# Kernel optimization log

Hardware: AMD Instinct MI355X
Metric: run time of the kernel (lower is better)

The kernel has to match this reference:

```python
import jax, jax.numpy as jnp
import numpy as np

N_HEAD = 16
D_MODEL = 1024
D_HEAD = D_MODEL // N_HEAD  # 64
B, S = 1, 4096


def setup_inputs() -> dict:
    key = jax.random.key(0)
    ks = jax.random.split(key, 7)
    q = jax.random.normal(ks[0], (B, S, D_MODEL), dtype=jnp.float32)
    k = jax.random.normal(ks[1], (B, S, D_MODEL), dtype=jnp.float32)
    v = jax.random.normal(ks[2], (B, S, D_MODEL), dtype=jnp.float32)
    mask = jnp.ones((S, S), dtype=bool)
    # params match torch.rand init (uniform [0,1)); use uniform here too
    w_q = jax.random.uniform(ks[3], (D_MODEL, D_MODEL), dtype=jnp.float32)
    w_k = jax.random.uniform(ks[4], (D_HEAD, D_MODEL), dtype=jnp.float32)
    w_v = jax.random.uniform(ks[5], (D_HEAD, D_MODEL), dtype=jnp.float32)
    w_out = jax.random.uniform(ks[6], (D_MODEL, D_MODEL), dtype=jnp.float32)
    return {"q": q, "k": k, "v": v, "mask": mask,
            "w_q": w_q, "w_k": w_k, "w_v": w_v, "w_out": w_out}


def reference(q, k, v, mask, w_q, w_k, w_v, w_out):
    # F.linear(x, W) == x @ W.T
    query = q @ w_q.T                      # [b, n, d_model]
    key = k @ w_k.T                        # [b, s, d_head]  (single shared KV head)
    value = v @ w_v.T                      # [b, s, d_head]
    b, n, _ = query.shape
    query = query.reshape(b, n, N_HEAD, D_HEAD).transpose(0, 2, 1, 3)  # b h n d
    scores = jnp.einsum('bhnd,bsd->bhns', query, key) / jnp.sqrt(jnp.float32(D_HEAD))
    scores = jnp.where(mask[None, None], scores, jnp.float32(-jnp.inf))
    attn = jax.nn.softmax(scores, axis=-1)             # [b, h, n, s]
    out = jnp.einsum('bhns,bsd->bhnd', attn, value)    # [b, h, n, d]
    out = out.transpose(0, 2, 1, 3).reshape(b, n, D_MODEL)
    return out @ w_out.T
```

## Files before the change

kernel.cpp:

```cpp
#include <hip/hip_runtime.h>
#include <cstdint>
#include <cstddef>

#define S_LEN   4096
#define DM      1024
#define NHEAD   16
#define DH      64

typedef short bf16x8 __attribute__((ext_vector_type(8)));
typedef _Float16 f16x8 __attribute__((ext_vector_type(8)));
typedef float f32x4  __attribute__((ext_vector_type(4)));

__device__ __forceinline__ unsigned short f2bf(float x) {
    uint32_t u = __float_as_uint(x);
    u += 0x7fffu + ((u >> 16) & 1u);
    return (unsigned short)(u >> 16);
}
__device__ __forceinline__ float bf2f(unsigned short u) {
    return __uint_as_float(((uint32_t)u) << 16);
}
__device__ __forceinline__ unsigned pack_bf2(float a, float b) {
    return (unsigned)f2bf(a) | ((unsigned)f2bf(b) << 16);
}
__device__ __forceinline__ unsigned short f2h(float x) {
    _Float16 h = (_Float16)x;
    return __builtin_bit_cast(unsigned short, h);
}
__device__ __forceinline__ unsigned pack_h2(float a, float b) {
    return __builtin_bit_cast(unsigned, __builtin_amdgcn_cvt_pkrtz(a, b));
}
__device__ __forceinline__ void gl_lds16(const unsigned short* g, unsigned short* l) {
    __builtin_amdgcn_global_load_lds(
        (const __attribute__((address_space(1))) unsigned int*)g,
        (__attribute__((address_space(3))) unsigned int*)l, 16, 0, 0);
}

__global__ void cvt_all(const float* __restrict__ q, const float* __restrict__ k,
                        const float* __restrict__ v, const float* __restrict__ wq,
                        const float* __restrict__ wk, const float* __restrict__ wv,
                        const float* __restrict__ wo,
                        unsigned short* __restrict__ qh, unsigned short* __restrict__ ql,
                        unsigned short* __restrict__ kh, unsigned short* __restrict__ kl,
                        unsigned short* __restrict__ vh,
                        unsigned short* __restrict__ wqh, unsigned short* __restrict__ wql,
                        unsigned short* __restrict__ wkh, unsigned short* __restrict__ wkl,
                        unsigned short* __restrict__ wvh, unsigned short* __restrict__ woh)
{
    const int G1 = 1048576, GW = 262144, GK = 16384;
    int i = blockIdx.x * blockDim.x + threadIdx.x;
    const float* src; unsigned short* h; unsigned short* l = nullptr; int off;
    if (i < 3 * G1) {
        if (i < G1)            { src = q; h = qh; l = ql; off = i; }
        else if (i < 2 * G1)   { src = k; h = kh; l = kl; off = i - G1; }
        else                   { src = v; h = vh;         off = i - 2 * G1; }
    } else {
        int j = i - 3 * G1;
        if (j < GW)            { src = wq; h = wqh; l = wql; off = j; }
        else if (j < GW + GK)  { src = wk; h = wkh; l = wkl; off = j - GW; }
        else if (j < GW + 2*GK){ src = wv; h = wvh;          off = j - GW - GK; }
        else                   { src = wo; h = woh;          off = j - GW - 2 * GK; }
    }
    float4 vv = reinterpret_cast<const float4*>(src)[off];
    ushort4 hh;
    hh.x = f2bf(vv.x); hh.y = f2bf(vv.y); hh.z = f2bf(vv.z); hh.w = f2bf(vv.w);
    reinterpret_cast<ushort4*>(h)[off] = hh;
    if (l) {
        ushort4 ll;
        ll.x = f2bf(vv.x - bf2f(hh.x)); ll.y = f2bf(vv.y - bf2f(hh.y));
        ll.z = f2bf(vv.z - bf2f(hh.z)); ll.w = f2bf(vv.w - bf2f(hh.w));
        reinterpret_cast<ushort4*>(l)[off] = ll;
    }
}

template<int TERMS, int MODE>
__launch_bounds__(256)
__global__ void gemm_bt(const unsigned short* __restrict__ Ah,
                        const unsigned short* __restrict__ Al,
                        const unsigned short* __restrict__ Bh,
                        const unsigned short* __restrict__ Bl,
                        unsigned short* __restrict__ Ch,
                        unsigned short* __restrict__ Cl,
                        float* __restrict__ Cf,
                        int M, int N, int K, int ldc)
{
    __shared__ unsigned short As_h[64][72];
    __shared__ unsigned short Bs_h[64][72];
    __shared__ unsigned short As_l[TERMS == 3 ? 64 : 1][72];
    __shared__ unsigned short Bs_l[TERMS == 3 ? 64 : 1][72];

    const int tid  = threadIdx.x;
    const int wave = tid >> 6;
    const int lane = tid & 63;
    const int lm   = lane & 15;
    const int quad = lane >> 4;
    const int m0   = blockIdx.x * 64;
    const int n0   = blockIdx.y * 64;

    f32x4 acc[4] = {};

    for (int kc = 0; kc < K; kc += 64) {
#pragma unroll
        for (int i = 0; i < 2; ++i) {
            int c   = tid + i * 256;
            int r   = c >> 3;
            int col = (c & 7) * 8;
            *(uint4*)&As_h[r][col] = *(const uint4*)&Ah[(size_t)(m0 + r) * K + kc + col];
            *(uint4*)&Bs_h[r][col] = *(const uint4*)&Bh[(size_t)(n0 + r) * K + kc + col];
            if (TERMS == 3) {
                *(uint4*)&As_l[r][col] = *(const uint4*)&Al[(size_t)(m0 + r) * K + kc + col];
                *(uint4*)&Bs_l[r][col] = *(const uint4*)&Bl[(size_t)(n0 + r) * K + kc + col];
            }
        }
        __syncthreads();
#pragma unroll
        for (int kk = 0; kk < 64; kk += 32) {
            bf16x8 bh = *(const bf16x8*)&Bs_h[wave * 16 + lm][kk + quad * 8];
            bf16x8 bl;
            if (TERMS == 3) bl = *(const bf16x8*)&Bs_l[wave * 16 + lm][kk + quad * 8];
#pragma unroll
            for (int ms = 0; ms < 4; ++ms) {
                bf16x8 ah = *(const bf16x8*)&As_h[ms * 16 + lm][kk + quad * 8];
                acc[ms] = __builtin_amdgcn_mfma_f32_16x16x32_bf16(ah, bh, acc[ms], 0, 0, 0);
                if (TERMS == 3) {
                    bf16x8 al = *(const bf16x8*)&As_l[ms * 16 + lm][kk + quad * 8];
                    acc[ms] = __builtin_amdgcn_mfma_f32_16x16x32_bf16(ah, bl, acc[ms], 0, 0, 0);
                    acc[ms] = __builtin_amdgcn_mfma_f32_16x16x32_bf16(al, bh, acc[ms], 0, 0, 0);
                }
            }
        }
        __syncthreads();
    }

#pragma unroll
    for (int ms = 0; ms < 4; ++ms) {
#pragma unroll
        for (int r = 0; r < 4; ++r) {
            int row = m0 + ms * 16 + quad * 4 + r;
            int col = n0 + wave * 16 + lm;
            float v = acc[ms][r];
            if (MODE == 0) {
                unsigned short h = f2bf(v);
                Ch[(size_t)row * ldc + col] = h;
                Cl[(size_t)row * ldc + col] = f2bf(v - bf2f(h));
            } else if (MODE == 2) {
                Cf[(size_t)row * ldc + col] = v;
            } else if (MODE == 3) {
                Ch[(size_t)row * ldc + col] = f2h(v);
            } else if (MODE == 4) {
                Ch[(size_t)col * ldc + row] = f2h(v);
            }
        }
    }
}

template<int TERMS, int MODE>
__launch_bounds__(256)
__global__ void gemm_big(const unsigned short* __restrict__ Ah,
                         const unsigned short* __restrict__ Al,
                         const unsigned short* __restrict__ Bh,
                         const unsigned short* __restrict__ Bl,
                         unsigned short* __restrict__ Ch,
                         unsigned short* __restrict__ Cl,
                         float* __restrict__ Cf,
                         int M, int N, int K, int ldc)
{
    __shared__ unsigned short As_h[2][8192];
    __shared__ unsigned short Bs_h[2][8192];
    __shared__ unsigned short As_l[TERMS == 3 ? 2 : 1][TERMS == 3 ? 8192 : 1];
    __shared__ unsigned short Bs_l[TERMS == 3 ? 2 : 1][TERMS == 3 ? 8192 : 1];

    const int tid  = threadIdx.x;
    const int wave = tid >> 6;
    const int lane = tid & 63;
    const int lm   = lane & 15;
    const int quad = lane >> 4;
    const int wm   = wave >> 1;
    const int wn   = wave & 1;
    const int m0   = blockIdx.x * 128;
    const int n0   = blockIdx.y * 128;

    int srow[4], scol[4];
#pragma unroll
    for (int i = 0; i < 4; ++i) {
        int f = i * 256 + tid;
        srow[i] = f >> 3;
        scol[i] = ((f & 7) ^ (srow[i] & 7)) * 8;
    }

    auto stage = [&](int b, int kc) {
#pragma unroll
        for (int i = 0; i < 4; ++i) {
            const int dst = (i * 256 + wave * 64) * 8;
            gl_lds16(&Ah[(size_t)(m0 + srow[i]) * K + kc + scol[i]], &As_h[b][dst]);
            gl_lds16(&Bh[(size_t)(n0 + srow[i]) * K + kc + scol[i]], &Bs_h[b][dst]);
            if (TERMS == 3) {
                gl_lds16(&Al[(size_t)(m0 + srow[i]) * K + kc + scol[i]], &As_l[b][dst]);
                gl_lds16(&Bl[(size_t)(n0 + srow[i]) * K + kc + scol[i]], &Bs_l[b][dst]);
            }
        }
    };

    stage(0, 0);

    f32x4 acc[4][4] = {};
    const int nkc = K / 64;

    for (int it = 0; it < nkc; ++it) {
        const int b = it & 1;
        __syncthreads();
        if (it + 1 < nkc) stage(b ^ 1, (it + 1) * 64);

#pragma unroll
        for (int kk = 0; kk < 2; ++kk) {
            bf16x8 bh[4], bl[4];
#pragma unroll
            for (int ns = 0; ns < 4; ++ns) {
                const int off = (wn * 64 + ns * 16 + lm) * 64 + ((kk * 4 + quad) ^ (lm & 7)) * 8;
                bh[ns] = *(const bf16x8*)&Bs_h[b][off];
                if (TERMS == 3) bl[ns] = *(const bf16x8*)&Bs_l[b][off];
            }
#pragma unroll
            for (int ms = 0; ms < 4; ++ms) {
                const int off = (wm * 64 + ms * 16 + lm) * 64 + ((kk * 4 + quad) ^ (lm & 7)) * 8;
                bf16x8 ah = *(const bf16x8*)&As_h[b][off];
                bf16x8 al;
                if (TERMS == 3) al = *(const bf16x8*)&As_l[b][off];
#pragma unroll
                for (int ns = 0; ns < 4; ++ns) {
                    acc[ms][ns] = __builtin_amdgcn_mfma_f32_16x16x32_bf16(ah, bh[ns], acc[ms][ns], 0, 0, 0);
                    if (TERMS == 3) {
                        acc[ms][ns] = __builtin_amdgcn_mfma_f32_16x16x32_bf16(ah, bl[ns], acc[ms][ns], 0, 0, 0);
                        acc[ms][ns] = __builtin_amdgcn_mfma_f32_16x16x32_bf16(al, bh[ns], acc[ms][ns], 0, 0, 0);
                    }
                }
            }
        }
    }

#pragma unroll
    for (int ms = 0; ms < 4; ++ms)
#pragma unroll
        for (int ns = 0; ns < 4; ++ns)
#pragma unroll
            for (int r = 0; r < 4; ++r) {
                int row = m0 + wm * 64 + ms * 16 + quad * 4 + r;
                int col = n0 + wn * 64 + ns * 16 + lm;
                float v = acc[ms][ns][r];
                if (MODE == 0) {
                    unsigned short h = f2bf(v);
                    Ch[(size_t)row * ldc + col] = h;
                    Cl[(size_t)row * ldc + col] = f2bf(v - bf2f(h));
                } else if (MODE == 2) {
                    Cf[(size_t)row * ldc + col] = v;
                } else if (MODE == 3) {
                    Ch[(size_t)row * ldc + col] = f2h(v);
                }
            }
}

__launch_bounds__(256)
__global__ void flash_kernel(const unsigned short* __restrict__ Qf,
                             const unsigned short* __restrict__ Kf,
                             const unsigned short* __restrict__ Vt,
                             unsigned short* __restrict__ Op,
                             float* __restrict__ Mb,
                             float* __restrict__ Lb)
{
    __shared__ unsigned short Ks[2][4096];
    __shared__ unsigned short Vs[2][4096];

    const int tid  = threadIdx.x;
    const int wave = tid >> 6;
    const int lane = tid & 63;
    const int lm   = lane & 15;
    const int quad = lane >> 4;
    const int q0   = blockIdx.x * 128;
    const int h    = blockIdx.y;
    const int sp   = blockIdx.z;
    const int kbase = sp * (S_LEN / 2);
    const float c  = 0.125f * 1.44269504f;

    const int r0 = tid >> 3,         c0 = ((tid & 7) ^ (r0 & 7)) * 8;
    const int r1 = (tid + 256) >> 3, c1 = ((tid & 7) ^ (r1 & 7)) * 8;
    const int ldsA = wave * 512;
    const int ldsB = 2048 + wave * 512;

    auto stage = [&](int kt, int b) {
        gl_lds16(&Kf[(size_t)(kt + r0) * DH + c0], &Ks[b][ldsA]);
        gl_lds16(&Kf[(size_t)(kt + r1) * DH + c1], &Ks[b][ldsB]);
        gl_lds16(&Vt[(size_t)r0 * S_LEN + kt + c0], &Vs[b][ldsA]);
        gl_lds16(&Vt[(size_t)r1 * S_LEN + kt + c1], &Vs[b][ldsB]);
    };

    stage(kbase, 0);

    f16x8 qf[2][2];
#pragma unroll
    for (int nb = 0; nb < 2; ++nb)
#pragma unroll
        for (int kk = 0; kk < 2; ++kk) {
            size_t idx = (size_t)(q0 + wave * 32 + nb * 16 + lm) * DM + h * DH + kk * 32 + quad * 8;
            qf[nb][kk] = *(const f16x8*)&Qf[idx];
        }

    f32x4 oacc[2][4] = {};
    float m_run[2] = {-1e30f, -1e30f}, l_run[2] = {0.f, 0.f};

    for (int it = 0; it < 32; ++it) {
        const int b = it & 1;
        const int kt = kbase + it * 64;
        __syncthreads();
        if (it + 1 < 32) stage(kt + 64, b ^ 1);

        f32x4 sacc[2][4] = {};
#pragma unroll
        for (int kk = 0; kk < 2; ++kk) {
#pragma unroll
            for (int ms = 0; ms < 4; ++ms) {
                const int off = (ms * 16 + lm) * 64 + ((4 * kk + quad) ^ (lm & 7)) * 8;
                f16x8 kfr = *(const f16x8*)&Ks[b][off];
#pragma unroll
                for (int nb = 0; nb < 2; ++nb)
                    sacc[nb][ms] = __builtin_amdgcn_mfma_f32_16x16x32_f16(kfr, qf[nb][kk], sacc[nb][ms], 0, 0, 0);
            }
        }

        float mn[2];
#pragma unroll
        for (int nb = 0; nb < 2; ++nb) {
            float mx = -1e30f;
#pragma unroll
            for (int ms = 0; ms < 4; ++ms)
#pragma unroll
                for (int r = 0; r < 4; ++r) mx = fmaxf(mx, sacc[nb][ms][r]);
            mx = fmaxf(mx, __shfl_xor(mx, 16));
            mx = fmaxf(mx, __shfl_xor(mx, 32));
            mn[nb] = fmaxf(m_run[nb], mx);
        }

        if (__any((mn[0] > m_run[0]) || (mn[1] > m_run[1]))) {
#pragma unroll
            for (int mq = 0; mq < 2; ++mq) {
                float alpha = __builtin_amdgcn_exp2f((m_run[mq] - mn[mq]) * c);
                l_run[mq] *= alpha;
                m_run[mq] = mn[mq];
                float ar[4];
#pragma unroll
                for (int r = 0; r < 4; ++r) ar[r] = __shfl(alpha, quad * 4 + r);
#pragma unroll
                for (int nd = 0; nd < 4; ++nd)
#pragma unroll
                    for (int r = 0; r < 4; ++r) oacc[mq][nd][r] *= ar[r];
            }
        }

        unsigned pk[2][4][2];
#pragma unroll
        for (int nb = 0; nb < 2; ++nb) {
            float mc = m_run[nb] * c;
            float ps = 0.f;
#pragma unroll
            for (int ms = 0; ms < 4; ++ms) {
                float pr[4];
#pragma unroll
                for (int r = 0; r < 4; ++r) {
                    pr[r] = __builtin_amdgcn_exp2f(fmaf(sacc[nb][ms][r], c, -mc));
                    ps += pr[r];
                }
                pk[nb][ms][0] = pack_h2(pr[0], pr[1]);
                pk[nb][ms][1] = pack_h2(pr[2], pr[3]);
            }
            ps += __shfl_xor(ps, 16);
            ps += __shfl_xor(ps, 32);
            l_run[nb] += ps;
        }

#pragma unroll
        for (int kb = 0; kb < 2; ++kb) {
            f16x8 pa[2];
#pragma unroll
            for (int nb = 0; nb < 2; ++nb) {
                unsigned af[4] __attribute__((aligned(16)));
#pragma unroll
                for (int d = 0; d < 4; ++d) {
                    int srcl = ((2 * quad + (d >> 1)) & 3) * 16 + lm;
                    unsigned v_lo = (unsigned)__shfl((int)pk[nb][2 * kb][d & 1], srcl);
                    unsigned v_hi = (unsigned)__shfl((int)pk[nb][2 * kb + 1][d & 1], srcl);
                    af[d] = (quad < 2) ? v_lo : v_hi;
                }
                pa[nb] = *(f16x8*)af;
            }
#pragma unroll
            for (int nd = 0; nd < 4; ++nd) {
                const int off = (nd * 16 + lm) * 64 + ((4 * kb + quad) ^ (lm & 7)) * 8;
                f16x8 vb = *(const f16x8*)&Vs[b][off];
#pragma unroll
                for (int nb = 0; nb < 2; ++nb)
                    oacc[nb][nd] = __builtin_amdgcn_mfma_f32_16x16x32_f16(pa[nb], vb, oacc[nb][nd], 0, 0, 0);
            }
        }
    }

    unsigned short* Osp = Op + (size_t)sp * NHEAD * S_LEN * DH;
#pragma unroll
    for (int mq = 0; mq < 2; ++mq) {
#pragma unroll
        for (int nd = 0; nd < 4; ++nd)
#pragma unroll
            for (int r = 0; r < 4; ++r) {
                int q = q0 + wave * 32 + mq * 16 + quad * 4 + r;
                Osp[((size_t)h * S_LEN + q) * DH + nd * 16 + lm] = f2bf(oacc[mq][nd][r]);
            }
        if (quad == 0) {
            int q = q0 + wave * 32 + mq * 16 + lm;
            Mb[(size_t)sp * NHEAD * S_LEN + h * S_LEN + q] = m_run[mq];
            Lb[(size_t)sp * NHEAD * S_LEN + h * S_LEN + q] = l_run[mq];
        }
    }
}

__global__ void merge_kernel(const unsigned short* __restrict__ Op,
                             const float* __restrict__ Mb,
                             const float* __restrict__ Lb,
                             unsigned short* __restrict__ O)
{
    const float c = 0.125f * 1.44269504f;
    int i = blockIdx.x * blockDim.x + threadIdx.x;
    int hq = i >> 5;
    int dp = i & 31;
    int h = hq >> 12, qq = hq & 4095;
    const unsigned* o1 = (const unsigned*)Op;
    const unsigned* o2 = (const unsigned*)(Op + (size_t)NHEAD * S_LEN * DH);
    float m1 = Mb[hq], m2 = Mb[NHEAD * S_LEN + hq];
    float l1 = Lb[hq], l2 = Lb[NHEAD * S_LEN + hq];
    float ms = fmaxf(m1, m2);
    float w1 = __builtin_amdgcn_exp2f((m1 - ms) * c);
    float w2 = __builtin_amdgcn_exp2f((m2 - ms) * c);
    float inv = 1.0f / (l1 * w1 + l2 * w2);
    unsigned u1 = o1[i], u2 = o2[i];
    float a = (bf2f(u1 & 0xffff) * w1 + bf2f(u2 & 0xffff) * w2) * inv;
    float b = (bf2f(u1 >> 16)    * w1 + bf2f(u2 >> 16)    * w2) * inv;
    ((unsigned*)O)[(size_t)qq * (DM / 2) + h * (DH / 2) + dp] = pack_bf2(a, b);
}

extern "C" void kernel_launch(void* const* d_in, const int* in_sizes, int n_in,
                              void* d_out, int out_size, void* d_ws, size_t ws_size,
                              hipStream_t stream)
{
    (void)in_sizes; (void)n_in; (void)out_size; (void)ws_size;
    const float* q     = (const float*)d_in[0];
    const float* k     = (const float*)d_in[1];
    const float* v     = (const float*)d_in[2];
    const float* w_q   = (const float*)d_in[4];
    const float* w_k   = (const float*)d_in[5];
    const float* w_v   = (const float*)d_in[6];
    const float* w_out = (const float*)d_in[7];
    float* out = (float*)d_out;

    char* ws = (char*)d_ws;
    size_t off = 0;
    auto alloc = [&](size_t bytes) -> unsigned short* {
        unsigned short* p = (unsigned short*)(ws + off);
        off += (bytes + 255) & ~(size_t)255;
        return p;
    };
    const size_t SZ_QKV = (size_t)S_LEN * DM * 2;
    const size_t SZ_WQ  = (size_t)DM * DM * 2;
    const size_t SZ_WK  = (size_t)DH * DM * 2;
    const size_t SZ_KV  = (size_t)S_LEN * DH * 2;

    unsigned short* qh  = alloc(SZ_QKV);
    unsigned short* ql  = alloc(SZ_QKV);
    unsigned short* kh  = alloc(SZ_QKV);
    unsigned short* kl  = alloc(SZ_QKV);
    unsigned short* vh  = alloc(SZ_QKV);
    unsigned short* wqh = alloc(SZ_WQ);
    unsigned short* wql = alloc(SZ_WQ);
    unsigned short* wkh = alloc(SZ_WK);
    unsigned short* wkl = alloc(SZ_WK);
    unsigned short* wvh = alloc(SZ_WK);
    unsigned short* woh = alloc(SZ_WQ);
    unsigned short* Qf  = alloc(SZ_QKV);
    unsigned short* Kf  = alloc(SZ_KV);
    unsigned short* Vtf = alloc(SZ_KV);
    unsigned short* obf = qh;

    unsigned short* Op = kh;
    float* Mb = (float*)vh;
    float* Lb = Mb + 2 * NHEAD * S_LEN;

    cvt_all<<<dim3(14464), 256, 0, stream>>>(q, k, v, w_q, w_k, w_v, w_out,
                                             qh, ql, kh, kl, vh,
                                             wqh, wql, wkh, wkl, wvh, woh);

    gemm_big<3, 3><<<dim3(32, 8), 256, 0, stream>>>(qh, ql, wqh, wql, Qf, nullptr, nullptr,
                                                    S_LEN, DM, DM, DM);
    gemm_bt<3, 3><<<dim3(64, 1), 256, 0, stream>>>(kh, kl, wkh, wkl, Kf, nullptr, nullptr,
                                                   S_LEN, DH, DM, DH);
    gemm_bt<1, 4><<<dim3(64, 1), 256, 0, stream>>>(vh, nullptr, wvh, nullptr, Vtf, nullptr, nullptr,
                                                   S_LEN, DH, DM, S_LEN);

    flash_kernel<<<dim3(32, 16, 2), 256, 0, stream>>>(Qf, Kf, Vtf, Op, Mb, Lb);
    merge_kernel<<<dim3(8192), 256, 0, stream>>>(Op, Mb, Lb, obf);

    gemm_big<1, 2><<<dim3(32, 8), 256, 0, stream>>>(obf, nullptr, woh, nullptr, nullptr, nullptr, out,
                                                    S_LEN, DM, DM, DM);
}
```

Measured before the change: 383.9 us.

## Load K/V fragments directly from global into registers, drop LDS staging

Removes the shared-memory double buffer and __syncthreads in the flash attention kernel. Each wave now loads its K and V MFMA fragments straight from global memory (relying on L1/L2 caching, since all waves read the same tiles), with K prefetched one iteration ahead in a register ping-pong. Launch bounds are raised to target two blocks per SIMD for occupancy. This removes barrier and LDS traffic but multiplies global/L2 loads by the number of waves and increases register pressure.

```diff
diff --git a/kernel.cpp b/kernel.cpp
--- a/kernel.cpp
+++ b/kernel.cpp
@@ -258,7 +258,7 @@
             }
 }
 
-__launch_bounds__(256)
+__launch_bounds__(256, 2)
 __global__ void flash_kernel(const unsigned short* __restrict__ Qf,
                              const unsigned short* __restrict__ Kf,
                              const unsigned short* __restrict__ Vt,
@@ -266,9 +266,6 @@
                              float* __restrict__ Mb,
                              float* __restrict__ Lb)
 {
-    __shared__ unsigned short Ks[2][4096];
-    __shared__ unsigned short Vs[2][4096];
-
     const int tid  = threadIdx.x;
     const int wave = tid >> 6;
     const int lane = tid & 63;
@@ -280,20 +277,6 @@
     const int kbase = sp * (S_LEN / 2);
     const float c  = 0.125f * 1.44269504f;
 
-    const int r0 = tid >> 3,         c0 = ((tid & 7) ^ (r0 & 7)) * 8;
-    const int r1 = (tid + 256) >> 3, c1 = ((tid & 7) ^ (r1 & 7)) * 8;
-    const int ldsA = wave * 512;
-    const int ldsB = 2048 + wave * 512;
-
-    auto stage = [&](int kt, int b) {
-        gl_lds16(&Kf[(size_t)(kt + r0) * DH + c0], &Ks[b][ldsA]);
-        gl_lds16(&Kf[(size_t)(kt + r1) * DH + c1], &Ks[b][ldsB]);
-        gl_lds16(&Vt[(size_t)r0 * S_LEN + kt + c0], &Vs[b][ldsA]);
-        gl_lds16(&Vt[(size_t)r1 * S_LEN + kt + c1], &Vs[b][ldsB]);
-    };
-
-    stage(kbase, 0);
-
     f16x8 qf[2][2];
 #pragma unroll
     for (int nb = 0; nb < 2; ++nb)
@@ -306,24 +289,32 @@
     f32x4 oacc[2][4] = {};
     float m_run[2] = {-1e30f, -1e30f}, l_run[2] = {0.f, 0.f};
 
-    for (int it = 0; it < 32; ++it) {
-        const int b = it & 1;
+    auto load_k = [&](f16x8 (&kf)[2][4], int kt) {
+#pragma unroll
+        for (int kk = 0; kk < 2; ++kk)
+#pragma unroll
+            for (int ms = 0; ms < 4; ++ms)
+                kf[kk][ms] = *(const f16x8*)&Kf[(size_t)(kt + ms * 16 + lm) * DH + kk * 32 + quad * 8];
+    };
+
+    auto body = [&](f16x8 (&kc)[2][4], f16x8 (&kn)[2][4], int it) {
         const int kt = kbase + it * 64;
-        __syncthreads();
-        if (it + 1 < 32) stage(kt + 64, b ^ 1);
+        load_k(kn, kbase + (it + 1 < 32 ? it + 1 : 31) * 64);
+        f16x8 vfr[2][4];
+#pragma unroll
+        for (int kb = 0; kb < 2; ++kb)
+#pragma unroll
+            for (int nd = 0; nd < 4; ++nd)
+                vfr[kb][nd] = *(const f16x8*)&Vt[(size_t)(nd * 16 + lm) * S_LEN + kt + kb * 32 + quad * 8];
 
         f32x4 sacc[2][4] = {};
 #pragma unroll
-        for (int kk = 0; kk < 2; ++kk) {
-#pragma unroll
-            for (int ms = 0; ms < 4; ++ms) {
-                const int off = (ms * 16 + lm) * 64 + ((4 * kk + quad) ^ (lm & 7)) * 8;
-                f16x8 kfr = *(const f16x8*)&Ks[b][off];
+        for (int kk = 0; kk < 2; ++kk)
+#pragma unroll
+            for (int ms = 0; ms < 4; ++ms)
 #pragma unroll
                 for (int nb = 0; nb < 2; ++nb)
-                    sacc[nb][ms] = __builtin_amdgcn_mfma_f32_16x16x32_f16(kfr, qf[nb][kk], sacc[nb][ms], 0, 0, 0);
-            }
-        }
+                    sacc[nb][ms] = __builtin_amdgcn_mfma_f32_16x16x32_f16(kc[kk][ms], qf[nb][kk], sacc[nb][ms], 0, 0, 0);
 
         float mn[2];
 #pragma unroll
@@ -391,14 +382,19 @@
                 pa[nb] = *(f16x8*)af;
             }
 #pragma unroll
-            for (int nd = 0; nd < 4; ++nd) {
-                const int off = (nd * 16 + lm) * 64 + ((4 * kb + quad) ^ (lm & 7)) * 8;
-                f16x8 vb = *(const f16x8*)&Vs[b][off];
+            for (int nd = 0; nd < 4; ++nd)
 #pragma unroll
                 for (int nb = 0; nb < 2; ++nb)
-                    oacc[nb][nd] = __builtin_amdgcn_mfma_f32_16x16x32_f16(pa[nb], vb, oacc[nb][nd], 0, 0, 0);
-            }
-        }
+                    oacc[nb][nd] = __builtin_amdgcn_mfma_f32_16x16x32_f16(pa[nb], vfr[kb][nd], oacc[nb][nd], 0, 0, 0);
+        }
+    };
+
+    f16x8 kfA[2][4], kfB[2][4];
+    load_k(kfA, kbase);
+#pragma unroll 1
+    for (int jt = 0; jt < 16; ++jt) {
+        body(kfA, kfB, 2 * jt);
+        body(kfB, kfA, 2 * jt + 1);
     }
 
     unsigned short* Osp = Op + (size_t)sp * NHEAD * S_LEN * DH;
```

Measured after the change: 480.1 us. 1.25x slower.

## Fuse fp32-to-bf16 split into KV projection and merge into output projection

Applied to the files above, without the earlier changes.

The K/V projections now read the fp32 inputs directly and split them into bf16 hi/lo inside the GEMM tile load, so the k/v conversion passes and their intermediate buffers are gone. The flash-split merge is folded into a new output-projection GEMM that combines the two partial outputs while staging the A tile. This drops one kernel launch and several full-size intermediate writes and reads. In exchange, the output projection uses a smaller 64x64 tile kernel instead of the double-buffered big GEMM, and the KV kernel does conversion arithmetic in its load path.

```diff
diff --git a/kernel.cpp b/kernel.cpp
--- a/kernel.cpp
+++ b/kernel.cpp
@@ -34,32 +34,31 @@
         (const __attribute__((address_space(1))) unsigned int*)g,
         (__attribute__((address_space(3))) unsigned int*)l, 16, 0, 0);
 }
-
-__global__ void cvt_all(const float* __restrict__ q, const float* __restrict__ k,
-                        const float* __restrict__ v, const float* __restrict__ wq,
-                        const float* __restrict__ wk, const float* __restrict__ wv,
-                        const float* __restrict__ wo,
-                        unsigned short* __restrict__ qh, unsigned short* __restrict__ ql,
-                        unsigned short* __restrict__ kh, unsigned short* __restrict__ kl,
-                        unsigned short* __restrict__ vh,
-                        unsigned short* __restrict__ wqh, unsigned short* __restrict__ wql,
-                        unsigned short* __restrict__ wkh, unsigned short* __restrict__ wkl,
-                        unsigned short* __restrict__ wvh, unsigned short* __restrict__ woh)
+__device__ __forceinline__ void split8(const float4& a0, const float4& a1,
+                                       ushort4& h0, ushort4& h1,
+                                       ushort4& l0, ushort4& l1) {
+    h0.x = f2bf(a0.x); l0.x = f2bf(a0.x - bf2f(h0.x));
+    h0.y = f2bf(a0.y); l0.y = f2bf(a0.y - bf2f(h0.y));
+    h0.z = f2bf(a0.z); l0.z = f2bf(a0.z - bf2f(h0.z));
+    h0.w = f2bf(a0.w); l0.w = f2bf(a0.w - bf2f(h0.w));
+    h1.x = f2bf(a1.x); l1.x = f2bf(a1.x - bf2f(h1.x));
+    h1.y = f2bf(a1.y); l1.y = f2bf(a1.y - bf2f(h1.y));
+    h1.z = f2bf(a1.z); l1.z = f2bf(a1.z - bf2f(h1.z));
+    h1.w = f2bf(a1.w); l1.w = f2bf(a1.w - bf2f(h1.w));
+}
+
+__global__ void cvt_qw(const float* __restrict__ q, const float* __restrict__ wq,
+                       const float* __restrict__ wo,
+                       unsigned short* __restrict__ qh, unsigned short* __restrict__ ql,
+                       unsigned short* __restrict__ wqh, unsigned short* __restrict__ wql,
+                       unsigned short* __restrict__ woh)
 {
-    const int G1 = 1048576, GW = 262144, GK = 16384;
+    const int G1 = 1048576, GW = 262144;
     int i = blockIdx.x * blockDim.x + threadIdx.x;
     const float* src; unsigned short* h; unsigned short* l = nullptr; int off;
-    if (i < 3 * G1) {
-        if (i < G1)            { src = q; h = qh; l = ql; off = i; }
-        else if (i < 2 * G1)   { src = k; h = kh; l = kl; off = i - G1; }
-        else                   { src = v; h = vh;         off = i - 2 * G1; }
-    } else {
-        int j = i - 3 * G1;
-        if (j < GW)            { src = wq; h = wqh; l = wql; off = j; }
-        else if (j < GW + GK)  { src = wk; h = wkh; l = wkl; off = j - GW; }
-        else if (j < GW + 2*GK){ src = wv; h = wvh;          off = j - GW - GK; }
-        else                   { src = wo; h = woh;          off = j - GW - 2 * GK; }
-    }
+    if (i < G1)            { src = q;  h = qh;  l = ql;  off = i; }
+    else if (i < G1 + GW)  { src = wq; h = wqh; l = wql; off = i - G1; }
+    else                   { src = wo; h = woh;          off = i - G1 - GW; }
     float4 vv = reinterpret_cast<const float4*>(src)[off];
     ushort4 hh;
     hh.x = f2bf(vv.x); hh.y = f2bf(vv.y); hh.z = f2bf(vv.z); hh.w = f2bf(vv.w);
@@ -72,21 +71,15 @@
     }
 }
 
-template<int TERMS, int MODE>
 __launch_bounds__(256)
-__global__ void gemm_bt(const unsigned short* __restrict__ Ah,
-                        const unsigned short* __restrict__ Al,
-                        const unsigned short* __restrict__ Bh,
-                        const unsigned short* __restrict__ Bl,
-                        unsigned short* __restrict__ Ch,
-                        unsigned short* __restrict__ Cl,
-                        float* __restrict__ Cf,
-                        int M, int N, int K, int ldc)
+__global__ void kv_proj(const float* __restrict__ kin, const float* __restrict__ vin,
+                        const float* __restrict__ wk, const float* __restrict__ wv,
+                        unsigned short* __restrict__ Kf, unsigned short* __restrict__ Vtf)
 {
     __shared__ unsigned short As_h[64][72];
     __shared__ unsigned short Bs_h[64][72];
-    __shared__ unsigned short As_l[TERMS == 3 ? 64 : 1][72];
-    __shared__ unsigned short Bs_l[TERMS == 3 ? 64 : 1][72];
+    __shared__ unsigned short As_l[64][72];
+    __shared__ unsigned short Bs_l[64][72];
 
     const int tid  = threadIdx.x;
     const int wave = tid >> 6;
@@ -94,80 +87,73 @@
     const int lm   = lane & 15;
     const int quad = lane >> 4;
     const int m0   = blockIdx.x * 64;
-    const int n0   = blockIdx.y * 64;
+    const bool isK = (blockIdx.y == 0);
+    const float* A = isK ? kin : vin;
+    const float* B = isK ? wk : wv;
 
     f32x4 acc[4] = {};
 
-    for (int kc = 0; kc < K; kc += 64) {
+    for (int kc = 0; kc < DM; kc += 64) {
+        __syncthreads();
 #pragma unroll
         for (int i = 0; i < 2; ++i) {
             int c   = tid + i * 256;
             int r   = c >> 3;
             int col = (c & 7) * 8;
-            *(uint4*)&As_h[r][col] = *(const uint4*)&Ah[(size_t)(m0 + r) * K + kc + col];
-            *(uint4*)&Bs_h[r][col] = *(const uint4*)&Bh[(size_t)(n0 + r) * K + kc + col];
-            if (TERMS == 3) {
-                *(uint4*)&As_l[r][col] = *(const uint4*)&Al[(size_t)(m0 + r) * K + kc + col];
-                *(uint4*)&Bs_l[r][col] = *(const uint4*)&Bl[(size_t)(n0 + r) * K + kc + col];
-            }
+            float4 a0 = *(const float4*)&A[(size_t)(m0 + r) * DM + kc + col];
+            float4 a1 = *(const float4*)&A[(size_t)(m0 + r) * DM + kc + col + 4];
+            float4 b0 = *(const float4*)&B[(size_t)r * DM + kc + col];
+            float4 b1 = *(const float4*)&B[(size_t)r * DM + kc + col + 4];
+            ushort4 h0, h1, l0, l1;
+            split8(a0, a1, h0, h1, l0, l1);
+            *(ushort4*)&As_h[r][col] = h0;  *(ushort4*)&As_h[r][col + 4] = h1;
+            if (isK) { *(ushort4*)&As_l[r][col] = l0;  *(ushort4*)&As_l[r][col + 4] = l1; }
+            split8(b0, b1, h0, h1, l0, l1);
+            *(ushort4*)&Bs_h[r][col] = h0;  *(ushort4*)&Bs_h[r][col + 4] = h1;
+            if (isK) { *(ushort4*)&Bs_l[r][col] = l0;  *(ushort4*)&Bs_l[r][col + 4] = l1; }
         }
         __syncthreads();
 #pragma unroll
         for (int kk = 0; kk < 64; kk += 32) {
             bf16x8 bh = *(const bf16x8*)&Bs_h[wave * 16 + lm][kk + quad * 8];
             bf16x8 bl;
-            if (TERMS == 3) bl = *(const bf16x8*)&Bs_l[wave * 16 + lm][kk + quad * 8];
+            if (isK) bl = *(const bf16x8*)&Bs_l[wave * 16 + lm][kk + quad * 8];
 #pragma unroll
             for (int ms = 0; ms < 4; ++ms) {
                 bf16x8 ah = *(const bf16x8*)&As_h[ms * 16 + lm][kk + quad * 8];
                 acc[ms] = __builtin_amdgcn_mfma_f32_16x16x32_bf16(ah, bh, acc[ms], 0, 0, 0);
-                if (TERMS == 3) {
+                if (isK) {
                     bf16x8 al = *(const bf16x8*)&As_l[ms * 16 + lm][kk + quad * 8];
                     acc[ms] = __builtin_amdgcn_mfma_f32_16x16x32_bf16(ah, bl, acc[ms], 0, 0, 0);
                     acc[ms] = __builtin_amdgcn_mfma_f32_16x16x32_bf16(al, bh, acc[ms], 0, 0, 0);
                 }
             }
         }
-        __syncthreads();
-    }
-
-#pragma unroll
-    for (int ms = 0; ms < 4; ++ms) {
+    }
+
+#pragma unroll
+    for (int ms = 0; ms < 4; ++ms)
 #pragma unroll
         for (int r = 0; r < 4; ++r) {
             int row = m0 + ms * 16 + quad * 4 + r;
-            int col = n0 + wave * 16 + lm;
-            float v = acc[ms][r];
-            if (MODE == 0) {
-                unsigned short h = f2bf(v);
-                Ch[(size_t)row * ldc + col] = h;
-                Cl[(size_t)row * ldc + col] = f2bf(v - bf2f(h));
-            } else if (MODE == 2) {
-                Cf[(size_t)row * ldc + col] = v;
-            } else if (MODE == 3) {
-                Ch[(size_t)row * ldc + col] = f2h(v);
-            } else if (MODE == 4) {
-                Ch[(size_t)col * ldc + row] = f2h(v);
-            }
-        }
-    }
-}
-
-template<int TERMS, int MODE>
+            int col = wave * 16 + lm;
+            if (isK) Kf[(size_t)row * DH + col] = f2h(acc[ms][r]);
+            else     Vtf[(size_t)col * S_LEN + row] = f2h(acc[ms][r]);
+        }
+}
+
 __launch_bounds__(256)
 __global__ void gemm_big(const unsigned short* __restrict__ Ah,
                          const unsigned short* __restrict__ Al,
                          const unsigned short* __restrict__ Bh,
                          const unsigned short* __restrict__ Bl,
                          unsigned short* __restrict__ Ch,
-                         unsigned short* __restrict__ Cl,
-                         float* __restrict__ Cf,
                          int M, int N, int K, int ldc)
 {
     __shared__ unsigned short As_h[2][8192];
     __shared__ unsigned short Bs_h[2][8192];
-    __shared__ unsigned short As_l[TERMS == 3 ? 2 : 1][TERMS == 3 ? 8192 : 1];
-    __shared__ unsigned short Bs_l[TERMS == 3 ? 2 : 1][TERMS == 3 ? 8192 : 1];
+    __shared__ unsigned short As_l[2][8192];
+    __shared__ unsigned short Bs_l[2][8192];
 
     const int tid  = threadIdx.x;
     const int wave = tid >> 6;
@@ -193,10 +179,8 @@
             const int dst = (i * 256 + wave * 64) * 8;
             gl_lds16(&Ah[(size_t)(m0 + srow[i]) * K + kc + scol[i]], &As_h[b][dst]);
             gl_lds16(&Bh[(size_t)(n0 + srow[i]) * K + kc + scol[i]], &Bs_h[b][dst]);
-            if (TERMS == 3) {
-                gl_lds16(&Al[(size_t)(m0 + srow[i]) * K + kc + scol[i]], &As_l[b][dst]);
-                gl_lds16(&Bl[(size_t)(n0 + srow[i]) * K + kc + scol[i]], &Bs_l[b][dst]);
-            }
+            gl_lds16(&Al[(size_t)(m0 + srow[i]) * K + kc + scol[i]], &As_l[b][dst]);
+            gl_lds16(&Bl[(size_t)(n0 + srow[i]) * K + kc + scol[i]], &Bs_l[b][dst]);
         }
     };
 
@@ -217,21 +201,18 @@
             for (int ns = 0; ns < 4; ++ns) {
                 const int off = (wn * 64 + ns * 16 + lm) * 64 + ((kk * 4 + quad) ^ (lm & 7)) * 8;
                 bh[ns] = *(const bf16x8*)&Bs_h[b][off];
-                if (TERMS == 3) bl[ns] = *(const bf16x8*)&Bs_l[b][off];
+                bl[ns] = *(const bf16x8*)&Bs_l[b][off];
             }
 #pragma unroll
             for (int ms = 0; ms < 4; ++ms) {
                 const int off = (wm * 64 + ms * 16 + lm) * 64 + ((kk * 4 + quad) ^ (lm & 7)) * 8;
                 bf16x8 ah = *(const bf16x8*)&As_h[b][off];
-                bf16x8 al;
-                if (TERMS == 3) al = *(const bf16x8*)&As_l[b][off];
+                bf16x8 al = *(const bf16x8*)&As_l[b][off];
 #pragma unroll
                 for (int ns = 0; ns < 4; ++ns) {
                     acc[ms][ns] = __builtin_amdgcn_mfma_f32_16x16x32_bf16(ah, bh[ns], acc[ms][ns], 0, 0, 0);
-                    if (TERMS == 3) {
-                        acc[ms][ns] = __builtin_amdgcn_mfma_f32_16x16x32_bf16(ah, bl[ns], acc[ms][ns], 0, 0, 0);
-                        acc[ms][ns] = __builtin_amdgcn_mfma_f32_16x16x32_bf16(al, bh[ns], acc[ms][ns], 0, 0, 0);
-                    }
+                    acc[ms][ns] = __builtin_amdgcn_mfma_f32_16x16x32_bf16(ah, bl[ns], acc[ms][ns], 0, 0, 0);
+                    acc[ms][ns] = __builtin_amdgcn_mfma_f32_16x16x32_bf16(al, bh[ns], acc[ms][ns], 0, 0, 0);
                 }
             }
         }
@@ -245,16 +226,7 @@
             for (int r = 0; r < 4; ++r) {
                 int row = m0 + wm * 64 + ms * 16 + quad * 4 + r;
                 int col = n0 + wn * 64 + ns * 16 + lm;
-                float v = acc[ms][ns][r];
-                if (MODE == 0) {
-                    unsigned short h = f2bf(v);
-                    Ch[(size_t)row * ldc + col] = h;
-                    Cl[(size_t)row * ldc + col] = f2bf(v - bf2f(h));
-                } else if (MODE == 2) {
-                    Cf[(size_t)row * ldc + col] = v;
-                } else if (MODE == 3) {
-                    Ch[(size_t)row * ldc + col] = f2h(v);
-                }
+                Ch[(size_t)row * ldc + col] = f2h(acc[ms][ns][r]);
             }
 }
 
@@ -419,28 +391,82 @@
     }
 }
 
-__global__ void merge_kernel(const unsigned short* __restrict__ Op,
-                             const float* __restrict__ Mb,
-                             const float* __restrict__ Lb,
-                             unsigned short* __restrict__ O)
+__launch_bounds__(256)
+__global__ void out_proj(const unsigned short* __restrict__ Op,
+                         const float* __restrict__ Mb,
+                         const float* __restrict__ Lb,
+                         const unsigned short* __restrict__ Wo,
+                         float* __restrict__ out)
 {
-    const float c = 0.125f * 1.44269504f;
-    int i = blockIdx.x * blockDim.x + threadIdx.x;
-    int hq = i >> 5;
-    int dp = i & 31;
-    int h = hq >> 12, qq = hq & 4095;
-    const unsigned* o1 = (const unsigned*)Op;
-    const unsigned* o2 = (const unsigned*)(Op + (size_t)NHEAD * S_LEN * DH);
-    float m1 = Mb[hq], m2 = Mb[NHEAD * S_LEN + hq];
-    float l1 = Lb[hq], l2 = Lb[NHEAD * S_LEN + hq];
-    float ms = fmaxf(m1, m2);
-    float w1 = __builtin_amdgcn_exp2f((m1 - ms) * c);
-    float w2 = __builtin_amdgcn_exp2f((m2 - ms) * c);
-    float inv = 1.0f / (l1 * w1 + l2 * w2);
-    unsigned u1 = o1[i], u2 = o2[i];
-    float a = (bf2f(u1 & 0xffff) * w1 + bf2f(u2 & 0xffff) * w2) * inv;
-    float b = (bf2f(u1 >> 16)    * w1 + bf2f(u2 >> 16)    * w2) * inv;
-    ((unsigned*)O)[(size_t)qq * (DM / 2) + h * (DH / 2) + dp] = pack_bf2(a, b);
+    __shared__ unsigned short As[64][72];
+    __shared__ unsigned short Bs[64][72];
+
+    const int tid  = threadIdx.x;
+    const int wave = tid >> 6;
+    const int lane = tid & 63;
+    const int lm   = lane & 15;
+    const int quad = lane >> 4;
+    const int m0   = blockIdx.x * 64;
+    const int n0   = blockIdx.y * 64;
+    const float c  = 0.125f * 1.44269504f;
+    const int HS   = NHEAD * S_LEN;
+    const size_t OSP = (size_t)NHEAD * S_LEN * DH;
+
+    f32x4 acc[4] = {};
+
+    for (int it = 0; it < 16; ++it) {
+        __syncthreads();
+#pragma unroll
+        for (int i = 0; i < 2; ++i) {
+            int cc  = tid + i * 256;
+            int r   = cc >> 3;
+            int col = (cc & 7) * 8;
+            int q   = m0 + r;
+            int hq  = it * S_LEN + q;
+            float m1 = Mb[hq], m2 = Mb[HS + hq];
+            float l1 = Lb[hq], l2 = Lb[HS + hq];
+            float mm = fmaxf(m1, m2);
+            float w1 = __builtin_amdgcn_exp2f((m1 - mm) * c);
+            float w2 = __builtin_amdgcn_exp2f((m2 - mm) * c);
+            float inv = 1.0f / (l1 * w1 + l2 * w2);
+            w1 *= inv; w2 *= inv;
+            size_t base = ((size_t)it * S_LEN + q) * DH + col;
+            uint4 u1 = *(const uint4*)&Op[base];
+            uint4 u2 = *(const uint4*)&Op[OSP + base];
+            unsigned mrg[4];
+            const unsigned* p1 = (const unsigned*)&u1;
+            const unsigned* p2 = (const unsigned*)&u2;
+#pragma unroll
+            for (int d = 0; d < 4; ++d) {
+                float a = bf2f((unsigned short)(p1[d] & 0xffff)) * w1
+                        + bf2f((unsigned short)(p2[d] & 0xffff)) * w2;
+                float b = bf2f((unsigned short)(p1[d] >> 16)) * w1
+                        + bf2f((unsigned short)(p2[d] >> 16)) * w2;
+                mrg[d] = pack_bf2(a, b);
+            }
+            *(uint4*)&As[r][col] = *(uint4*)mrg;
+            *(uint4*)&Bs[r][col] = *(const uint4*)&Wo[(size_t)(n0 + r) * DM + it * 64 + col];
+        }
+        __syncthreads();
+#pragma unroll
+        for (int kk = 0; kk < 64; kk += 32) {
+            bf16x8 bh = *(const bf16x8*)&Bs[wave * 16 + lm][kk + quad * 8];
+#pragma unroll
+            for (int ms = 0; ms < 4; ++ms) {
+                bf16x8 ah = *(const bf16x8*)&As[ms * 16 + lm][kk + quad * 8];
+                acc[ms] = __builtin_amdgcn_mfma_f32_16x16x32_bf16(ah, bh, acc[ms], 0, 0, 0);
+            }
+        }
+    }
+
+#pragma unroll
+    for (int ms = 0; ms < 4; ++ms)
+#pragma unroll
+        for (int r = 0; r < 4; ++r) {
+            int row = m0 + ms * 16 + quad * 4 + r;
+            int col = n0 + wave * 16 + lm;
+            out[(size_t)row * DM + col] = acc[ms][r];
+        }
 }
 
 extern "C" void kernel_launch(void* const* d_in, const int* in_sizes, int n_in,
@@ -466,43 +492,27 @@
     };
     const size_t SZ_QKV = (size_t)S_LEN * DM * 2;
     const size_t SZ_WQ  = (size_t)DM * DM * 2;
-    const size_t SZ_WK  = (size_t)DH * DM * 2;
     const size_t SZ_KV  = (size_t)S_LEN * DH * 2;
 
     unsigned short* qh  = alloc(SZ_QKV);
     unsigned short* ql  = alloc(SZ_QKV);
-    unsigned short* kh  = alloc(SZ_QKV);
-    unsigned short* kl  = alloc(SZ_QKV);
-    unsigned short* vh  = alloc(SZ_QKV);
     unsigned short* wqh = alloc(SZ_WQ);
     unsigned short* wql = alloc(SZ_WQ);
-    unsigned short* wkh = alloc(SZ_WK);
-    unsigned short* wkl = alloc(SZ_WK);
-    unsigned short* wvh = alloc(SZ_WK);
     unsigned short* woh = alloc(SZ_WQ);
     unsigned short* Qf  = alloc(SZ_QKV);
     unsigned short* Kf  = alloc(SZ_KV);
     unsigned short* Vtf = alloc(SZ_KV);
-    unsigned short* obf = qh;
-
-    unsigned short* Op = kh;
-    float* Mb = (float*)vh;
-    float* Lb = Mb + 2 * NHEAD * S_LEN;
-
-    cvt_all<<<dim3(14464), 256, 0, stream>>>(q, k, v, w_q, w_k, w_v, w_out,
-                                             qh, ql, kh, kl, vh,
-                                             wqh, wql, wkh, wkl, wvh, woh);
-
-    gemm_big<3, 3><<<dim3(32, 8), 256, 0, stream>>>(qh, ql, wqh, wql, Qf, nullptr, nullptr,
-                                                    S_LEN, DM, DM, DM);
-    gemm_bt<3, 3><<<dim3(64, 1), 256, 0, stream>>>(kh, kl, wkh, wkl, Kf, nullptr, nullptr,
-                                                   S_LEN, DH, DM, DH);
-    gemm_bt<1, 4><<<dim3(64, 1), 256, 0, stream>>>(vh, nullptr, wvh, nullptr, Vtf, nullptr, nullptr,
-                                                   S_LEN, DH, DM, S_LEN);
+    unsigned short* Op  = alloc(2 * NHEAD * SZ_KV);
+    float* Mb = (float*)alloc(2 * NHEAD * S_LEN * 4);
+    float* Lb = (float*)alloc(2 * NHEAD * S_LEN * 4);
+
+    kv_proj<<<dim3(64, 2), 256, 0, stream>>>(k, v, w_k, w_v, Kf, Vtf);
+
+    cvt_qw<<<dim3(6144), 256, 0, stream>>>(q, w_q, w_out, qh, ql, wqh, wql, woh);
+
+    gemm_big<<<dim3(32, 8), 256, 0, stream>>>(qh, ql, wqh, wql, Qf, S_LEN, DM, DM, DM);
 
     flash_kernel<<<dim3(32, 16, 2), 256, 0, stream>>>(Qf, Kf, Vtf, Op, Mb, Lb);
-    merge_kernel<<<dim3(8192), 256, 0, stream>>>(Op, Mb, Lb, obf);
-
-    gemm_big<1, 2><<<dim3(32, 8), 256, 0, stream>>>(obf, nullptr, woh, nullptr, nullptr, nullptr, out,
-                                                    S_LEN, DM, DM, DM);
-}
+
+    out_proj<<<dim3(64, 16), 256, 0, stream>>>(Op, Mb, Lb, woh, out);
+}
```

Result: no change. 376.8 us (-1.9%).
